# Optimization experiments

Hardware: AMD Instinct MI355X
Metric: run time of the kernel (lower is better)

## Reference

```python
import jax, jax.numpy as jnp
import numpy as np

WS = 8          # window size
NH = 8          # num heads
DIM = 256
HD = DIM // NH  # head dim = 32
SCALE = HD ** -0.5
EPS = 1e-5


def _rel_pos_index(ws):
    # deterministic int index buffer, same math as the torch __init__
    coords = jnp.stack(jnp.meshgrid(jnp.arange(ws), jnp.arange(ws), indexing='ij'))  # [2,ws,ws]
    cf = coords.reshape(2, -1)                     # [2, N]
    rel = cf[:, :, None] - cf[:, None, :]          # [2, N, N]
    return (rel[0] + ws - 1) * (2 * ws - 1) + (rel[1] + ws - 1)  # [N, N]


def _ln(h, g, b):
    m = jnp.mean(h, axis=-1, keepdims=True)
    v = jnp.mean((h - m) ** 2, axis=-1, keepdims=True)
    return (h - m) / jnp.sqrt(v + EPS) * g + b


def setup_inputs() -> dict:
    key = jax.random.key(0)
    ks = jax.random.split(key, 16)
    B_, N, D = 4096, WS * WS, DIM
    s = 0.02
    return {
        'x':      jax.random.normal(ks[0], (B_, N, D), jnp.float32),
        # enhanced qkv: Linear(D,2D) -> LN -> GELU -> Linear(2D,3D)
        'w_qkv1': jax.random.normal(ks[1], (D, 2 * D), jnp.float32) * s,
        'b_qkv1': jnp.zeros((2 * D,), jnp.float32),
        'g_qkv':  jnp.ones((2 * D,), jnp.float32),
        'be_qkv': jnp.zeros((2 * D,), jnp.float32),
        'w_qkv2': jax.random.normal(ks[2], (2 * D, 3 * D), jnp.float32) * s,
        'b_qkv2': jnp.zeros((3 * D,), jnp.float32),
        # relative position bias table [(2*WS-1)^2, NH]
        'rpb':    jax.random.normal(ks[3], ((2 * WS - 1) ** 2, NH), jnp.float32) * s,
        # enhanced proj: Linear(D,2D) -> LN -> GELU -> Linear(2D,D)
        'w_p1':   jax.random.normal(ks[4], (D, 2 * D), jnp.float32) * s,
        'b_p1':   jnp.zeros((2 * D,), jnp.float32),
        'g_p':    jnp.ones((2 * D,), jnp.float32),
        'be_p':   jnp.zeros((2 * D,), jnp.float32),
        'w_p2':   jax.random.normal(ks[5], (2 * D, D), jnp.float32) * s,
        'b_p2':   jnp.zeros((D,), jnp.float32),
    }


def reference(x, w_qkv1, b_qkv1, g_qkv, be_qkv, w_qkv2, b_qkv2, rpb,
              w_p1, b_p1, g_p, be_p, w_p2, b_p2):
    B_, N, C = x.shape
    # enhanced QKV chain: Linear -> LayerNorm -> GELU -> Linear
    h = jax.nn.gelu(_ln(x @ w_qkv1 + b_qkv1, g_qkv, be_qkv), approximate=False)
    qkv = h @ w_qkv2 + b_qkv2                              # [B_, N, 3C]
    qkv = qkv.reshape(B_, N, 3, NH, HD).transpose(2, 0, 3, 1, 4)  # [3, B_, H, N, hd]
    q, k, v = qkv[0], qkv[1], qkv[2]
    attn = jnp.einsum('bhnd,bhmd->bhnm', q * SCALE, k)     # [B_, H, N, N]
    idx = _rel_pos_index(WS)                                # [N, N] int
    bias = rpb[idx.reshape(-1)].reshape(N, N, NH).transpose(2, 0, 1)  # [H, N, N]
    attn = jax.nn.softmax(attn + bias[None], axis=-1)
    out = jnp.einsum('bhnm,bhmd->bhnd', attn, v)           # [B_, H, N, hd]
    out = out.transpose(0, 2, 1, 3).reshape(B_, N, C)
    # enhanced proj chain: Linear -> LayerNorm -> GELU -> Linear
    h = jax.nn.gelu(_ln(out @ w_p1 + b_p1, g_p, be_p), approximate=False)
    return h @ w_p2 + b_p2
```

## Files before the change

### kernel.cpp

```cpp
#include <hip/hip_runtime.h>


typedef __bf16 bf16_t;
typedef __bf16 bf16x8 __attribute__((ext_vector_type(8)));
typedef __bf16 bf16x4 __attribute__((ext_vector_type(4)));
typedef float f32x4 __attribute__((ext_vector_type(4)));

__device__ __forceinline__ f32x4 mfma16(bf16x8 a, bf16x8 b, f32x4 acc) {
  return __builtin_amdgcn_mfma_f32_16x16x32_bf16(a, b, acc, 0, 0, 0);
}

#define SWZ(row, byteoff) ((byteoff) ^ (((row) & 7) << 4))

__device__ __forceinline__ float gelu_f(float v) {
  float e = __expf(v * (1.59576912f + 0.07135482f * v * v));
  return v - v * __builtin_amdgcn_rcpf(1.0f + e);
}

__global__ void wtrans_kernel(const float* __restrict__ src, bf16_t* __restrict__ dst,
                              int kshift, int N, int total) {
  int i = blockIdx.x * 256 + threadIdx.x;
  if (i >= total) return;
  int K = 1 << kshift;
  int k = i & (K - 1);
  int n = i >> kshift;
  dst[i] = (bf16_t)src[(size_t)k * N + n];
}

__global__ void biastab_kernel(const float* __restrict__ rpb, float* __restrict__ bt) {
  int e = blockIdx.x * 256 + threadIdx.x;
  int hd = e >> 12, i = (e >> 6) & 63, j = e & 63;
  int idx = ((i >> 3) - (j >> 3) + 7) * 15 + ((i & 7) - (j & 7) + 7);
  bt[e] = rpb[idx * 8 + hd];
}

__device__ __forceinline__ void gemmT_ln_gelu16(
    const char* bsrc, const bf16_t* __restrict__ wt,
    const float* __restrict__ bias, const float* __restrict__ gamma,
    const float* __restrict__ beta,
    char* dst, int flb, float2* part, int wave, int g, int c)
{
  f32x4 acc[2][4] = {};
#pragma unroll
  for (int kt = 0; kt < 8; ++kt) {
    bf16x8 a[2], b[4];
#pragma unroll
    for (int mt = 0; mt < 2; ++mt)
      a[mt] = *(const bf16x8*)(wt + (size_t)(wave * 32 + mt * 16 + c) * 256 + kt * 32 + g * 8);
#pragma unroll
    for (int nt = 0; nt < 4; ++nt) {
      int T = nt * 16 + c;
      b[nt] = *(const bf16x8*)(bsrc + SWZ(T, T * 512 + kt * 64 + g * 16));
    }
#pragma unroll
    for (int mt = 0; mt < 2; ++mt)
#pragma unroll
      for (int nt = 0; nt < 4; ++nt)
        acc[mt][nt] = mfma16(a[mt], b[nt], acc[mt][nt]);
  }
  float s[4] = {0.f, 0.f, 0.f, 0.f}, ss[4] = {0.f, 0.f, 0.f, 0.f};
#pragma unroll
  for (int mt = 0; mt < 2; ++mt) {
    float4 b4 = *(const float4*)(bias + wave * 32 + mt * 16 + g * 4);
#pragma unroll
    for (int nt = 0; nt < 4; ++nt)
#pragma unroll
      for (int r = 0; r < 4; ++r) {
        float v = acc[mt][nt][r] + ((const float*)&b4)[r];
        acc[mt][nt][r] = v;
        s[nt] += v;
        ss[nt] += v * v;
      }
  }
#pragma unroll
  for (int nt = 0; nt < 4; ++nt) {
    float sv = s[nt], ssv = ss[nt];
    sv += __shfl_xor(sv, 16, 64); ssv += __shfl_xor(ssv, 16, 64);
    sv += __shfl_xor(sv, 32, 64); ssv += __shfl_xor(ssv, 32, 64);
    if (g == 0) part[wave * 64 + nt * 16 + c] = make_float2(sv, ssv);
  }
  __syncthreads();
#pragma unroll
  for (int nt = 0; nt < 4; ++nt) {
    float sv = 0.f, ssv = 0.f;
#pragma unroll
    for (int w = 0; w < 16; ++w) {
      float2 p2 = part[w * 64 + nt * 16 + c];
      sv += p2.x; ssv += p2.y;
    }
    float m = sv * (1.f / 512.f);
    float rstd = rsqrtf(ssv * (1.f / 512.f) - m * m + 1e-5f);
#pragma unroll
    for (int mt = 0; mt < 2; ++mt)
#pragma unroll
      for (int r = 0; r < 4; ++r)
        acc[mt][nt][r] = (acc[mt][nt][r] - m) * rstd;
  }
#pragma unroll
  for (int mt = 0; mt < 2; ++mt) {
    float4 g4 = *(const float4*)(gamma + wave * 32 + mt * 16 + g * 4);
    float4 be4 = *(const float4*)(beta + wave * 32 + mt * 16 + g * 4);
    int f0 = flb + mt * 16 + g * 4;
#pragma unroll
    for (int nt = 0; nt < 4; ++nt) {
      int T = nt * 16 + c;
      bf16x4 h4;
#pragma unroll
      for (int r = 0; r < 4; ++r) {
        float v = acc[mt][nt][r] * ((const float*)&g4)[r] + ((const float*)&be4)[r];
        h4[r] = (bf16_t)gelu_f(v);
      }
      *(bf16x4*)(dst + SWZ(T, T * 512 + f0 * 2)) = h4;
    }
  }
}

__global__ __launch_bounds__(1024, 1) void g1qa_kernel(
    const float* __restrict__ x,
    const bf16_t* __restrict__ w1t, const float* __restrict__ b1,
    const float* __restrict__ gamma1, const float* __restrict__ beta1,
    const bf16_t* __restrict__ w2t, const float* __restrict__ b2,
    const float* __restrict__ bt,
    bf16_t* __restrict__ ao)
{
  __shared__ __align__(16) char sm[98304];
  char* rA = sm;
  char* rB = sm + 32768;
  float2* part = (float2*)(sm + 65536);
  const int tid = threadIdx.x;
  const int wave = tid >> 6, lane = tid & 63;
  const int g = lane >> 4, c = lane & 15;
  const int win = blockIdx.x;

  const float* xw = x + (size_t)win * 16384;
#pragma unroll
  for (int it = 0; it < 4; ++it) {
    int e = it * 4096 + tid * 4;
    float4 v = *(const float4*)(xw + e);
    int row = e >> 8, col = e & 255;
    bf16x4 t4;
    t4[0] = (bf16_t)v.x; t4[1] = (bf16_t)v.y; t4[2] = (bf16_t)v.z; t4[3] = (bf16_t)v.w;
    *(bf16x4*)(rA + SWZ(row, row * 512 + col * 2)) = t4;
  }
  __syncthreads();
  gemmT_ln_gelu16(rA, w1t, b1, gamma1, beta1, (wave < 8) ? rB : rA, (wave & 7) * 32,
                  part, wave, g, c);
  __syncthreads();

  const int hh = wave >> 1, mh = wave & 1;
  bf16x4 vreg[4], qreg[4], kreg[4];
  {
    f32x4 accv[4] = {}, accq[4] = {}, acck[4] = {};
    const bf16_t* wq = w2t + (size_t)(hh * 32 + mh * 16 + c) * 512;
    const bf16_t* wk = wq + (size_t)256 * 512;
    const bf16_t* wv = wq + (size_t)512 * 512;
#pragma unroll
    for (int kt = 0; kt < 16; ++kt) {
      const char* hb = (kt < 8) ? rB : rA;
      const int ko = (kt & 7) * 64 + g * 16;
      bf16x8 av = *(const bf16x8*)(wv + kt * 32 + g * 8);
      bf16x8 aq = *(const bf16x8*)(wq + kt * 32 + g * 8);
      bf16x8 ak = *(const bf16x8*)(wk + kt * 32 + g * 8);
      bf16x8 b[4];
#pragma unroll
      for (int nt = 0; nt < 4; ++nt) {
        int T = nt * 16 + c;
        b[nt] = *(const bf16x8*)(hb + SWZ(T, T * 512 + ko));
      }
#pragma unroll
      for (int nt = 0; nt < 4; ++nt) {
        accv[nt] = mfma16(av, b[nt], accv[nt]);
        accq[nt] = mfma16(aq, b[nt], accq[nt]);
        acck[nt] = mfma16(ak, b[nt], acck[nt]);
      }
    }
    float4 bv4 = *(const float4*)(b2 + 512 + hh * 32 + mh * 16 + g * 4);
    float4 bq4 = *(const float4*)(b2 + hh * 32 + mh * 16 + g * 4);
    float4 bk4 = *(const float4*)(b2 + 256 + hh * 32 + mh * 16 + g * 4);
#pragma unroll
    for (int nt = 0; nt < 4; ++nt)
#pragma unroll
      for (int r = 0; r < 4; ++r) {
        vreg[nt][r] = (bf16_t)(accv[nt][r] + ((const float*)&bv4)[r]);
        qreg[nt][r] = (bf16_t)((accq[nt][r] + ((const float*)&bq4)[r]) * 0.17677669529663687f);
        kreg[nt][r] = (bf16_t)(acck[nt][r] + ((const float*)&bk4)[r]);
      }
  }
  __syncthreads();

  {
    char* qb = sm + hh * 8192;
    const int d0 = mh * 16 + g * 4;
#pragma unroll
    for (int nt = 0; nt < 4; ++nt) {
      int T = nt * 16 + c;
      *(bf16x4*)(qb + SWZ(T, T * 64 + d0 * 2)) = qreg[nt];
      *(bf16x4*)(qb + 4096 + SWZ(T, T * 64 + d0 * 2)) = kreg[nt];
    }
    char* vs = sm + 65536 + hh * 4096;
#pragma unroll
    for (int nt = 0; nt < 4; ++nt) {
      int T = nt * 16 + c;
#pragma unroll
      for (int r = 0; r < 4; ++r) {
        int d = d0 + r;
        *(bf16_t*)(vs + SWZ(d, d * 128 + T * 2)) = vreg[nt][r];
      }
    }
  }
  __syncthreads();

  const int h8 = wave & 7, rowbase = (wave >> 3) * 32;
  char* qb = sm + h8 * 8192;
  char* vslot = sm + 65536 + h8 * 4096;
  const float* btab = bt + h8 * 4096;

  bf16x8 aq[2], bk[4];
#pragma unroll
  for (int mt = 0; mt < 2; ++mt) {
    int t = rowbase + mt * 16 + c;
    aq[mt] = *(const bf16x8*)(qb + SWZ(t, t * 64 + g * 16));
  }
#pragma unroll
  for (int nt = 0; nt < 4; ++nt) {
    int t = nt * 16 + c;
    bk[nt] = *(const bf16x8*)(qb + 4096 + SWZ(t, t * 64 + g * 16));
  }
  float p[2][4][4];
#pragma unroll
  for (int mt = 0; mt < 2; ++mt)
#pragma unroll
    for (int nt = 0; nt < 4; ++nt) {
      f32x4 z = {0.f, 0.f, 0.f, 0.f};
      f32x4 s4 = mfma16(aq[mt], bk[nt], z);
#pragma unroll
      for (int r = 0; r < 4; ++r) {
        int i = rowbase + mt * 16 + g * 4 + r, j = nt * 16 + c;
        p[mt][nt][r] = s4[r] + btab[i * 64 + j];
      }
    }
#pragma unroll
  for (int mt = 0; mt < 2; ++mt)
#pragma unroll
    for (int r = 0; r < 4; ++r) {
      float mx = fmaxf(fmaxf(p[mt][0][r], p[mt][1][r]), fmaxf(p[mt][2][r], p[mt][3][r]));
#pragma unroll
      for (int m = 1; m < 16; m <<= 1) mx = fmaxf(mx, __shfl_xor(mx, m, 64));
      float sum = 0.f;
#pragma unroll
      for (int nt = 0; nt < 4; ++nt) {
        float e = __expf(p[mt][nt][r] - mx);
        p[mt][nt][r] = e; sum += e;
      }
#pragma unroll
      for (int m = 1; m < 16; m <<= 1) sum += __shfl_xor(sum, m, 64);
      float rinv = 1.f / sum;
#pragma unroll
      for (int nt = 0; nt < 4; ++nt) p[mt][nt][r] *= rinv;
    }
  __syncthreads();

#pragma unroll
  for (int mt = 0; mt < 2; ++mt)
#pragma unroll
    for (int nt = 0; nt < 4; ++nt)
#pragma unroll
      for (int r = 0; r < 4; ++r) {
        int i = rowbase + mt * 16 + g * 4 + r, j = nt * 16 + c;
        *(bf16_t*)(qb + SWZ(i, i * 128 + j * 2)) = (bf16_t)p[mt][nt][r];
      }
  asm volatile("s_waitcnt lgkmcnt(0)" ::: "memory");
  f32x4 oacc[2][2] = {};
#pragma unroll
  for (int kp = 0; kp < 2; ++kp) {
    bf16x8 ap[2], bv[2];
#pragma unroll
    for (int mt = 0; mt < 2; ++mt) {
      int t = rowbase + mt * 16 + c;
      ap[mt] = *(const bf16x8*)(qb + SWZ(t, t * 128 + kp * 64 + g * 16));
    }
#pragma unroll
    for (int nt = 0; nt < 2; ++nt) {
      int d = nt * 16 + c;
      bv[nt] = *(const bf16x8*)(vslot + SWZ(d, d * 128 + kp * 64 + g * 16));
    }
#pragma unroll
    for (int mt = 0; mt < 2; ++mt)
#pragma unroll
      for (int nt = 0; nt < 2; ++nt)
        oacc[mt][nt] = mfma16(ap[mt], bv[nt], oacc[mt][nt]);
  }
#pragma unroll
  for (int mt = 0; mt < 2; ++mt)
#pragma unroll
    for (int nt = 0; nt < 2; ++nt)
#pragma unroll
      for (int r = 0; r < 4; ++r) {
        int T = rowbase + mt * 16 + g * 4 + r;
        ao[(size_t)(win * 64 + T) * 256 + h8 * 32 + nt * 16 + c] = (bf16_t)oacc[mt][nt][r];
      }
}

__global__ __launch_bounds__(1024, 1) void g3g4_kernel(
    const bf16_t* __restrict__ ao,
    const bf16_t* __restrict__ wp1t, const float* __restrict__ bp1,
    const float* __restrict__ gp, const float* __restrict__ bep,
    const bf16_t* __restrict__ wp2t, const float* __restrict__ bp2,
    float* __restrict__ out)
{
  __shared__ __align__(16) char sm[73728];
  char* rA = sm;
  char* rB = sm + 32768;
  float2* part = (float2*)(sm + 65536);
  const int tid = threadIdx.x;
  const int wave = tid >> 6, lane = tid & 63;
  const int g = lane >> 4, c = lane & 15;
  const int win = blockIdx.x;

  const bf16_t* aow = ao + (size_t)win * 16384;
#pragma unroll
  for (int it = 0; it < 2; ++it) {
    int e = it * 8192 + tid * 8;
    bf16x8 v = *(const bf16x8*)(aow + e);
    int row = e >> 8, col = e & 255;
    *(bf16x8*)(rA + SWZ(row, row * 512 + col * 2)) = v;
  }
  __syncthreads();
  gemmT_ln_gelu16(rA, wp1t, bp1, gp, bep, (wave < 8) ? rB : rA, (wave & 7) * 32,
                  part, wave, g, c);
  __syncthreads();

  f32x4 acc[4] = {};
#pragma unroll
  for (int kt = 0; kt < 16; ++kt) {
    const char* hb = (kt < 8) ? rB : rA;
    const int ko = (kt & 7) * 64 + g * 16;
    bf16x8 a = *(const bf16x8*)(wp2t + (size_t)(wave * 16 + c) * 512 + kt * 32 + g * 8);
    bf16x8 b[4];
#pragma unroll
    for (int nt = 0; nt < 4; ++nt) {
      int T = nt * 16 + c;
      b[nt] = *(const bf16x8*)(hb + SWZ(T, T * 512 + ko));
    }
#pragma unroll
    for (int nt = 0; nt < 4; ++nt)
      acc[nt] = mfma16(a, b[nt], acc[nt]);
  }
  float* ow = out + (size_t)win * 16384;
  float4 b4 = *(const float4*)(bp2 + wave * 16 + g * 4);
#pragma unroll
  for (int nt = 0; nt < 4; ++nt) {
    int T = nt * 16 + c;
    f32x4 o4;
#pragma unroll
    for (int r = 0; r < 4; ++r) o4[r] = acc[nt][r] + ((const float*)&b4)[r];
    *(f32x4*)(ow + T * 256 + wave * 16 + g * 4) = o4;
  }
}

extern "C" void kernel_launch(void* const* d_in, const int* in_sizes, int n_in,
                              void* d_out, int out_size, void* d_ws, size_t ws_size,
                              hipStream_t stream) {
  const float* x   = (const float*)d_in[0];
  const float* w1  = (const float*)d_in[1];
  const float* b1  = (const float*)d_in[2];
  const float* g1  = (const float*)d_in[3];
  const float* be1 = (const float*)d_in[4];
  const float* w2  = (const float*)d_in[5];
  const float* b2  = (const float*)d_in[6];
  const float* rpb = (const float*)d_in[7];
  const float* wp1 = (const float*)d_in[8];
  const float* bp1 = (const float*)d_in[9];
  const float* gp  = (const float*)d_in[10];
  const float* bep = (const float*)d_in[11];
  const float* wp2 = (const float*)d_in[12];
  const float* bp2 = (const float*)d_in[13];
  float* out = (float*)d_out;
  char* ws = (char*)d_ws;
  bf16_t* w1t  = (bf16_t*)(ws + 0);
  bf16_t* w2t  = (bf16_t*)(ws + 262144);
  bf16_t* wp1t = (bf16_t*)(ws + 1048576);
  bf16_t* wp2t = (bf16_t*)(ws + 1310720);
  float*  bt   = (float*)(ws + 1572864);
  bf16_t* ao   = (bf16_t*)(ws + 2097152);

  wtrans_kernel<<<512, 256, 0, stream>>>(w1, w1t, 8, 512, 131072);
  wtrans_kernel<<<1536, 256, 0, stream>>>(w2, w2t, 9, 768, 393216);
  wtrans_kernel<<<512, 256, 0, stream>>>(wp1, wp1t, 8, 512, 131072);
  wtrans_kernel<<<512, 256, 0, stream>>>(wp2, wp2t, 9, 256, 131072);
  biastab_kernel<<<128, 256, 0, stream>>>(rpb, bt);

  g1qa_kernel<<<4096, 1024, 0, stream>>>(x, w1t, b1, g1, be1, w2t, b2, bt, ao);
  g3g4_kernel<<<4096, 1024, 0, stream>>>(ao, wp1t, bp1, gp, bep, wp2t, bp2, out);
}
```

Before: 1.104 ms.

## Fuse attention and projection kernels into one per-window mega kernel

Merges the QKV+attention kernel and the projection-chain kernel into a single kernel per window. The attention output now stays in LDS (a new 32KB region) instead of round-tripping through global memory as bf16, and one launch is dropped. LDS use per block rises from 96KB to 128KB, which still allows one 1024-thread block per CU but may limit occupancy or scheduling flexibility.

```diff
diff --git a/kernel.cpp b/kernel.cpp
--- a/kernel.cpp
+++ b/kernel.cpp
@@ -115,18 +115,22 @@
   }
 }
 
-__global__ __launch_bounds__(1024, 1) void g1qa_kernel(
+__global__ __launch_bounds__(1024, 1) void mega_kernel(
     const float* __restrict__ x,
     const bf16_t* __restrict__ w1t, const float* __restrict__ b1,
     const float* __restrict__ gamma1, const float* __restrict__ beta1,
     const bf16_t* __restrict__ w2t, const float* __restrict__ b2,
     const float* __restrict__ bt,
-    bf16_t* __restrict__ ao)
+    const bf16_t* __restrict__ wp1t, const float* __restrict__ bp1,
+    const float* __restrict__ gp, const float* __restrict__ bep,
+    const bf16_t* __restrict__ wp2t, const float* __restrict__ bp2,
+    float* __restrict__ out)
 {
-  __shared__ __align__(16) char sm[98304];
+  __shared__ __align__(16) char sm[131072];
   char* rA = sm;
   char* rB = sm + 32768;
   float2* part = (float2*)(sm + 65536);
+  char* aoS = sm + 98304;
   const int tid = threadIdx.x;
   const int wave = tid >> 6, lane = tid & 63;
   const int g = lane >> 4, c = lane & 15;
@@ -210,151 +214,131 @@
   }
   __syncthreads();
 
-  const int h8 = wave & 7, rowbase = (wave >> 3) * 32;
-  char* qb = sm + h8 * 8192;
-  char* vslot = sm + 65536 + h8 * 4096;
-  const float* btab = bt + h8 * 4096;
-
-  bf16x8 aq[2], bk[4];
-#pragma unroll
-  for (int mt = 0; mt < 2; ++mt) {
-    int t = rowbase + mt * 16 + c;
-    aq[mt] = *(const bf16x8*)(qb + SWZ(t, t * 64 + g * 16));
-  }
-#pragma unroll
-  for (int nt = 0; nt < 4; ++nt) {
-    int t = nt * 16 + c;
-    bk[nt] = *(const bf16x8*)(qb + 4096 + SWZ(t, t * 64 + g * 16));
-  }
-  float p[2][4][4];
-#pragma unroll
-  for (int mt = 0; mt < 2; ++mt)
-#pragma unroll
-    for (int nt = 0; nt < 4; ++nt) {
-      f32x4 z = {0.f, 0.f, 0.f, 0.f};
-      f32x4 s4 = mfma16(aq[mt], bk[nt], z);
-#pragma unroll
-      for (int r = 0; r < 4; ++r) {
-        int i = rowbase + mt * 16 + g * 4 + r, j = nt * 16 + c;
-        p[mt][nt][r] = s4[r] + btab[i * 64 + j];
-      }
-    }
-#pragma unroll
-  for (int mt = 0; mt < 2; ++mt)
-#pragma unroll
-    for (int r = 0; r < 4; ++r) {
-      float mx = fmaxf(fmaxf(p[mt][0][r], p[mt][1][r]), fmaxf(p[mt][2][r], p[mt][3][r]));
-#pragma unroll
-      for (int m = 1; m < 16; m <<= 1) mx = fmaxf(mx, __shfl_xor(mx, m, 64));
-      float sum = 0.f;
-#pragma unroll
-      for (int nt = 0; nt < 4; ++nt) {
-        float e = __expf(p[mt][nt][r] - mx);
-        p[mt][nt][r] = e; sum += e;
-      }
-#pragma unroll
-      for (int m = 1; m < 16; m <<= 1) sum += __shfl_xor(sum, m, 64);
-      float rinv = 1.f / sum;
-#pragma unroll
-      for (int nt = 0; nt < 4; ++nt) p[mt][nt][r] *= rinv;
-    }
-  __syncthreads();
-
-#pragma unroll
-  for (int mt = 0; mt < 2; ++mt)
-#pragma unroll
-    for (int nt = 0; nt < 4; ++nt)
-#pragma unroll
-      for (int r = 0; r < 4; ++r) {
-        int i = rowbase + mt * 16 + g * 4 + r, j = nt * 16 + c;
-        *(bf16_t*)(qb + SWZ(i, i * 128 + j * 2)) = (bf16_t)p[mt][nt][r];
-      }
-  asm volatile("s_waitcnt lgkmcnt(0)" ::: "memory");
-  f32x4 oacc[2][2] = {};
-#pragma unroll
-  for (int kp = 0; kp < 2; ++kp) {
-    bf16x8 ap[2], bv[2];
+  {
+    const int h8 = wave & 7, rowbase = (wave >> 3) * 32;
+    char* qb = sm + h8 * 8192;
+    char* vslot = sm + 65536 + h8 * 4096;
+    const float* btab = bt + h8 * 4096;
+
+    bf16x8 aq[2], bk[4];
 #pragma unroll
     for (int mt = 0; mt < 2; ++mt) {
       int t = rowbase + mt * 16 + c;
-      ap[mt] = *(const bf16x8*)(qb + SWZ(t, t * 128 + kp * 64 + g * 16));
-    }
-#pragma unroll
-    for (int nt = 0; nt < 2; ++nt) {
-      int d = nt * 16 + c;
-      bv[nt] = *(const bf16x8*)(vslot + SWZ(d, d * 128 + kp * 64 + g * 16));
+      aq[mt] = *(const bf16x8*)(qb + SWZ(t, t * 64 + g * 16));
+    }
+#pragma unroll
+    for (int nt = 0; nt < 4; ++nt) {
+      int t = nt * 16 + c;
+      bk[nt] = *(const bf16x8*)(qb + 4096 + SWZ(t, t * 64 + g * 16));
+    }
+    float p[2][4][4];
+#pragma unroll
+    for (int mt = 0; mt < 2; ++mt)
+#pragma unroll
+      for (int nt = 0; nt < 4; ++nt) {
+        f32x4 z = {0.f, 0.f, 0.f, 0.f};
+        f32x4 s4 = mfma16(aq[mt], bk[nt], z);
+#pragma unroll
+        for (int r = 0; r < 4; ++r) {
+          int i = rowbase + mt * 16 + g * 4 + r, j = nt * 16 + c;
+          p[mt][nt][r] = s4[r] + btab[i * 64 + j];
+        }
+      }
+#pragma unroll
+    for (int mt = 0; mt < 2; ++mt)
+#pragma unroll
+      for (int r = 0; r < 4; ++r) {
+        float mx = fmaxf(fmaxf(p[mt][0][r], p[mt][1][r]), fmaxf(p[mt][2][r], p[mt][3][r]));
+#pragma unroll
+        for (int m = 1; m < 16; m <<= 1) mx = fmaxf(mx, __shfl_xor(mx, m, 64));
+        float sum = 0.f;
+#pragma unroll
+        for (int nt = 0; nt < 4; ++nt) {
+          float e = __expf(p[mt][nt][r] - mx);
+          p[mt][nt][r] = e; sum += e;
+        }
+#pragma unroll
+        for (int m = 1; m < 16; m <<= 1) sum += __shfl_xor(sum, m, 64);
+        float rinv = 1.f / sum;
+#pragma unroll
+        for (int nt = 0; nt < 4; ++nt) p[mt][nt][r] *= rinv;
+      }
+    __syncthreads();
+
+#pragma unroll
+    for (int mt = 0; mt < 2; ++mt)
+#pragma unroll
+      for (int nt = 0; nt < 4; ++nt)
+#pragma unroll
+        for (int r = 0; r < 4; ++r) {
+          int i = rowbase + mt * 16 + g * 4 + r, j = nt * 16 + c;
+          *(bf16_t*)(qb + SWZ(i, i * 128 + j * 2)) = (bf16_t)p[mt][nt][r];
+        }
+    asm volatile("s_waitcnt lgkmcnt(0)" ::: "memory");
+    f32x4 oacc[2][2] = {};
+#pragma unroll
+    for (int kp = 0; kp < 2; ++kp) {
+      bf16x8 ap[2], bv[2];
+#pragma unroll
+      for (int mt = 0; mt < 2; ++mt) {
+        int t = rowbase + mt * 16 + c;
+        ap[mt] = *(const bf16x8*)(qb + SWZ(t, t * 128 + kp * 64 + g * 16));
+      }
+#pragma unroll
+      for (int nt = 0; nt < 2; ++nt) {
+        int d = nt * 16 + c;
+        bv[nt] = *(const bf16x8*)(vslot + SWZ(d, d * 128 + kp * 64 + g * 16));
+      }
+#pragma unroll
+      for (int mt = 0; mt < 2; ++mt)
+#pragma unroll
+        for (int nt = 0; nt < 2; ++nt)
+          oacc[mt][nt] = mfma16(ap[mt], bv[nt], oacc[mt][nt]);
     }
 #pragma unroll
     for (int mt = 0; mt < 2; ++mt)
 #pragma unroll
       for (int nt = 0; nt < 2; ++nt)
-        oacc[mt][nt] = mfma16(ap[mt], bv[nt], oacc[mt][nt]);
-  }
-#pragma unroll
-  for (int mt = 0; mt < 2; ++mt)
-#pragma unroll
-    for (int nt = 0; nt < 2; ++nt)
-#pragma unroll
-      for (int r = 0; r < 4; ++r) {
-        int T = rowbase + mt * 16 + g * 4 + r;
-        ao[(size_t)(win * 64 + T) * 256 + h8 * 32 + nt * 16 + c] = (bf16_t)oacc[mt][nt][r];
-      }
-}
-
-__global__ __launch_bounds__(1024, 1) void g3g4_kernel(
-    const bf16_t* __restrict__ ao,
-    const bf16_t* __restrict__ wp1t, const float* __restrict__ bp1,
-    const float* __restrict__ gp, const float* __restrict__ bep,
-    const bf16_t* __restrict__ wp2t, const float* __restrict__ bp2,
-    float* __restrict__ out)
-{
-  __shared__ __align__(16) char sm[73728];
-  char* rA = sm;
-  char* rB = sm + 32768;
-  float2* part = (float2*)(sm + 65536);
-  const int tid = threadIdx.x;
-  const int wave = tid >> 6, lane = tid & 63;
-  const int g = lane >> 4, c = lane & 15;
-  const int win = blockIdx.x;
-
-  const bf16_t* aow = ao + (size_t)win * 16384;
-#pragma unroll
-  for (int it = 0; it < 2; ++it) {
-    int e = it * 8192 + tid * 8;
-    bf16x8 v = *(const bf16x8*)(aow + e);
-    int row = e >> 8, col = e & 255;
-    *(bf16x8*)(rA + SWZ(row, row * 512 + col * 2)) = v;
-  }
-  __syncthreads();
-  gemmT_ln_gelu16(rA, wp1t, bp1, gp, bep, (wave < 8) ? rB : rA, (wave & 7) * 32,
+#pragma unroll
+        for (int r = 0; r < 4; ++r) {
+          int T = rowbase + mt * 16 + g * 4 + r;
+          int f = h8 * 32 + nt * 16 + c;
+          *(bf16_t*)(aoS + SWZ(T, T * 512 + f * 2)) = (bf16_t)oacc[mt][nt][r];
+        }
+  }
+  __syncthreads();
+
+  gemmT_ln_gelu16(aoS, wp1t, bp1, gp, bep, (wave < 8) ? rB : rA, (wave & 7) * 32,
                   part, wave, g, c);
   __syncthreads();
 
-  f32x4 acc[4] = {};
-#pragma unroll
-  for (int kt = 0; kt < 16; ++kt) {
-    const char* hb = (kt < 8) ? rB : rA;
-    const int ko = (kt & 7) * 64 + g * 16;
-    bf16x8 a = *(const bf16x8*)(wp2t + (size_t)(wave * 16 + c) * 512 + kt * 32 + g * 8);
-    bf16x8 b[4];
-#pragma unroll
-    for (int nt = 0; nt < 4; ++nt) {
-      int T = nt * 16 + c;
-      b[nt] = *(const bf16x8*)(hb + SWZ(T, T * 512 + ko));
-    }
-#pragma unroll
-    for (int nt = 0; nt < 4; ++nt)
-      acc[nt] = mfma16(a, b[nt], acc[nt]);
-  }
-  float* ow = out + (size_t)win * 16384;
-  float4 b4 = *(const float4*)(bp2 + wave * 16 + g * 4);
-#pragma unroll
-  for (int nt = 0; nt < 4; ++nt) {
-    int T = nt * 16 + c;
-    f32x4 o4;
-#pragma unroll
-    for (int r = 0; r < 4; ++r) o4[r] = acc[nt][r] + ((const float*)&b4)[r];
-    *(f32x4*)(ow + T * 256 + wave * 16 + g * 4) = o4;
+  {
+    f32x4 acc[4] = {};
+#pragma unroll
+    for (int kt = 0; kt < 16; ++kt) {
+      const char* hb = (kt < 8) ? rB : rA;
+      const int ko = (kt & 7) * 64 + g * 16;
+      bf16x8 a = *(const bf16x8*)(wp2t + (size_t)(wave * 16 + c) * 512 + kt * 32 + g * 8);
+      bf16x8 b[4];
+#pragma unroll
+      for (int nt = 0; nt < 4; ++nt) {
+        int T = nt * 16 + c;
+        b[nt] = *(const bf16x8*)(hb + SWZ(T, T * 512 + ko));
+      }
+#pragma unroll
+      for (int nt = 0; nt < 4; ++nt)
+        acc[nt] = mfma16(a, b[nt], acc[nt]);
+    }
+    float* ow = out + (size_t)win * 16384;
+    float4 b4 = *(const float4*)(bp2 + wave * 16 + g * 4);
+#pragma unroll
+    for (int nt = 0; nt < 4; ++nt) {
+      int T = nt * 16 + c;
+      f32x4 o4;
+#pragma unroll
+      for (int r = 0; r < 4; ++r) o4[r] = acc[nt][r] + ((const float*)&b4)[r];
+      *(f32x4*)(ow + T * 256 + wave * 16 + g * 4) = o4;
+    }
   }
 }
 
@@ -382,7 +366,6 @@
   bf16_t* wp1t = (bf16_t*)(ws + 1048576);
   bf16_t* wp2t = (bf16_t*)(ws + 1310720);
   float*  bt   = (float*)(ws + 1572864);
-  bf16_t* ao   = (bf16_t*)(ws + 2097152);
 
   wtrans_kernel<<<512, 256, 0, stream>>>(w1, w1t, 8, 512, 131072);
   wtrans_kernel<<<1536, 256, 0, stream>>>(w2, w2t, 9, 768, 393216);
@@ -390,6 +373,6 @@
   wtrans_kernel<<<512, 256, 0, stream>>>(wp2, wp2t, 9, 256, 131072);
   biastab_kernel<<<128, 256, 0, stream>>>(rpb, bt);
 
-  g1qa_kernel<<<4096, 1024, 0, stream>>>(x, w1t, b1, g1, be1, w2t, b2, bt, ao);
-  g3g4_kernel<<<4096, 1024, 0, stream>>>(ao, wp1t, bp1, gp, bep, wp2t, bp2, out);
-}
+  mega_kernel<<<4096, 1024, 0, stream>>>(x, w1t, b1, g1, be1, w2t, b2, bt,
+                                         wp1t, bp1, gp, bep, wp2t, bp2, out);
+}
```

Measured after the change: 1.184 ms. 7.2% more time.

## Merge prep kernels, drop a barrier in QKV epilogue, retile final GEMM

Applied to the files above, without the earlier changes.

Folds the four weight-transpose launches and the bias-table launch into a single prep kernel to cut launch overhead. In the attention kernel, shared memory grows to 160KB so the Q/K/V results can be written directly into a fresh region, which removes a __syncthreads and the register staging of q/k/v. The final projection GEMM is retiled so each wave computes a 32x32 output tile instead of 16x64, reusing A and B fragments across two MFMAs each. The larger LDS footprint is still within one 1024-thread block per CU.

```diff
diff --git a/kernel.cpp b/kernel.cpp
--- a/kernel.cpp
+++ b/kernel.cpp
@@ -17,21 +17,42 @@
   return v - v * __builtin_amdgcn_rcpf(1.0f + e);
 }
 
-__global__ void wtrans_kernel(const float* __restrict__ src, bf16_t* __restrict__ dst,
-                              int kshift, int N, int total) {
+__global__ void prep_kernel(const float* __restrict__ w1, const float* __restrict__ w2,
+                            const float* __restrict__ wp1, const float* __restrict__ wp2,
+                            const float* __restrict__ rpb,
+                            bf16_t* __restrict__ w1t, bf16_t* __restrict__ w2t,
+                            bf16_t* __restrict__ wp1t, bf16_t* __restrict__ wp2t,
+                            float* __restrict__ bt) {
   int i = blockIdx.x * 256 + threadIdx.x;
-  if (i >= total) return;
-  int K = 1 << kshift;
-  int k = i & (K - 1);
-  int n = i >> kshift;
-  dst[i] = (bf16_t)src[(size_t)k * N + n];
-}
-
-__global__ void biastab_kernel(const float* __restrict__ rpb, float* __restrict__ bt) {
-  int e = blockIdx.x * 256 + threadIdx.x;
-  int hd = e >> 12, i = (e >> 6) & 63, j = e & 63;
-  int idx = ((i >> 3) - (j >> 3) + 7) * 15 + ((i & 7) - (j & 7) + 7);
-  bt[e] = rpb[idx * 8 + hd];
+  if (i < 131072) {
+    int k = i & 255, n = i >> 8;
+    w1t[i] = (bf16_t)w1[k * 512 + n];
+    return;
+  }
+  i -= 131072;
+  if (i < 393216) {
+    int k = i & 511, n = i >> 9;
+    w2t[i] = (bf16_t)w2[k * 768 + n];
+    return;
+  }
+  i -= 393216;
+  if (i < 131072) {
+    int k = i & 255, n = i >> 8;
+    wp1t[i] = (bf16_t)wp1[k * 512 + n];
+    return;
+  }
+  i -= 131072;
+  if (i < 131072) {
+    int k = i & 511, n = i >> 9;
+    wp2t[i] = (bf16_t)wp2[k * 256 + n];
+    return;
+  }
+  i -= 131072;
+  if (i < 32768) {
+    int hd = i >> 12, r = (i >> 6) & 63, j = i & 63;
+    int idx = ((r >> 3) - (j >> 3) + 7) * 15 + ((r & 7) - (j & 7) + 7);
+    bt[i] = rpb[idx * 8 + hd];
+  }
 }
 
 __device__ __forceinline__ void gemmT_ln_gelu16(
@@ -123,7 +144,7 @@
     const float* __restrict__ bt,
     bf16_t* __restrict__ ao)
 {
-  __shared__ __align__(16) char sm[98304];
+  __shared__ __align__(16) char sm[163840];
   char* rA = sm;
   char* rB = sm + 32768;
   float2* part = (float2*)(sm + 65536);
@@ -148,7 +169,6 @@
   __syncthreads();
 
   const int hh = wave >> 1, mh = wave & 1;
-  bf16x4 vreg[4], qreg[4], kreg[4];
   {
     f32x4 accv[4] = {}, accq[4] = {}, acck[4] = {};
     const bf16_t* wq = w2t + (size_t)(hh * 32 + mh * 16 + c) * 512;
@@ -177,42 +197,33 @@
     float4 bv4 = *(const float4*)(b2 + 512 + hh * 32 + mh * 16 + g * 4);
     float4 bq4 = *(const float4*)(b2 + hh * 32 + mh * 16 + g * 4);
     float4 bk4 = *(const float4*)(b2 + 256 + hh * 32 + mh * 16 + g * 4);
-#pragma unroll
-    for (int nt = 0; nt < 4; ++nt)
-#pragma unroll
-      for (int r = 0; r < 4; ++r) {
-        vreg[nt][r] = (bf16_t)(accv[nt][r] + ((const float*)&bv4)[r]);
-        qreg[nt][r] = (bf16_t)((accq[nt][r] + ((const float*)&bq4)[r]) * 0.17677669529663687f);
-        kreg[nt][r] = (bf16_t)(acck[nt][r] + ((const float*)&bk4)[r]);
-      }
-  }
-  __syncthreads();
-
-  {
-    char* qb = sm + hh * 8192;
+    char* qb = sm + 65536 + hh * 8192;
+    char* vs = sm + 131072 + hh * 4096;
     const int d0 = mh * 16 + g * 4;
 #pragma unroll
     for (int nt = 0; nt < 4; ++nt) {
       int T = nt * 16 + c;
-      *(bf16x4*)(qb + SWZ(T, T * 64 + d0 * 2)) = qreg[nt];
-      *(bf16x4*)(qb + 4096 + SWZ(T, T * 64 + d0 * 2)) = kreg[nt];
-    }
-    char* vs = sm + 65536 + hh * 4096;
-#pragma unroll
-    for (int nt = 0; nt < 4; ++nt) {
-      int T = nt * 16 + c;
+      bf16x4 q4, k4;
+#pragma unroll
+      for (int r = 0; r < 4; ++r) {
+        q4[r] = (bf16_t)((accq[nt][r] + ((const float*)&bq4)[r]) * 0.17677669529663687f);
+        k4[r] = (bf16_t)(acck[nt][r] + ((const float*)&bk4)[r]);
+      }
+      *(bf16x4*)(qb + SWZ(T, T * 64 + d0 * 2)) = q4;
+      *(bf16x4*)(qb + 4096 + SWZ(T, T * 64 + d0 * 2)) = k4;
 #pragma unroll
       for (int r = 0; r < 4; ++r) {
         int d = d0 + r;
-        *(bf16_t*)(vs + SWZ(d, d * 128 + T * 2)) = vreg[nt][r];
+        *(bf16_t*)(vs + SWZ(d, d * 128 + T * 2)) =
+            (bf16_t)(accv[nt][r] + ((const float*)&bv4)[r]);
       }
     }
   }
   __syncthreads();
 
   const int h8 = wave & 7, rowbase = (wave >> 3) * 32;
-  char* qb = sm + h8 * 8192;
-  char* vslot = sm + 65536 + h8 * 4096;
+  char* qb = sm + 65536 + h8 * 8192;
+  char* vslot = sm + 131072 + h8 * 4096;
   const float* btab = bt + h8 * 4096;
 
   bf16x8 aq[2], bk[4];
@@ -330,31 +341,41 @@
                   part, wave, g, c);
   __syncthreads();
 
-  f32x4 acc[4] = {};
-#pragma unroll
-  for (int kt = 0; kt < 16; ++kt) {
-    const char* hb = (kt < 8) ? rB : rA;
-    const int ko = (kt & 7) * 64 + g * 16;
-    bf16x8 a = *(const bf16x8*)(wp2t + (size_t)(wave * 16 + c) * 512 + kt * 32 + g * 8);
-    bf16x8 b[4];
-#pragma unroll
-    for (int nt = 0; nt < 4; ++nt) {
-      int T = nt * 16 + c;
-      b[nt] = *(const bf16x8*)(hb + SWZ(T, T * 512 + ko));
-    }
-#pragma unroll
-    for (int nt = 0; nt < 4; ++nt)
-      acc[nt] = mfma16(a, b[nt], acc[nt]);
-  }
-  float* ow = out + (size_t)win * 16384;
-  float4 b4 = *(const float4*)(bp2 + wave * 16 + g * 4);
-#pragma unroll
-  for (int nt = 0; nt < 4; ++nt) {
-    int T = nt * 16 + c;
-    f32x4 o4;
-#pragma unroll
-    for (int r = 0; r < 4; ++r) o4[r] = acc[nt][r] + ((const float*)&b4)[r];
-    *(f32x4*)(ow + T * 256 + wave * 16 + g * 4) = o4;
+  {
+    const int f0 = (wave & 7) * 32, t0 = (wave >> 3) * 32;
+    f32x4 acc[2][2] = {};
+#pragma unroll
+    for (int kt = 0; kt < 16; ++kt) {
+      const char* hb = (kt < 8) ? rB : rA;
+      const int ko = (kt & 7) * 64 + g * 16;
+      bf16x8 a[2], b[2];
+#pragma unroll
+      for (int mt = 0; mt < 2; ++mt)
+        a[mt] = *(const bf16x8*)(wp2t + (size_t)(f0 + mt * 16 + c) * 512 + kt * 32 + g * 8);
+#pragma unroll
+      for (int nt = 0; nt < 2; ++nt) {
+        int T = t0 + nt * 16 + c;
+        b[nt] = *(const bf16x8*)(hb + SWZ(T, T * 512 + ko));
+      }
+#pragma unroll
+      for (int mt = 0; mt < 2; ++mt)
+#pragma unroll
+        for (int nt = 0; nt < 2; ++nt)
+          acc[mt][nt] = mfma16(a[mt], b[nt], acc[mt][nt]);
+    }
+    float* ow = out + (size_t)win * 16384;
+#pragma unroll
+    for (int mt = 0; mt < 2; ++mt) {
+      float4 b4 = *(const float4*)(bp2 + f0 + mt * 16 + g * 4);
+#pragma unroll
+      for (int nt = 0; nt < 2; ++nt) {
+        int T = t0 + nt * 16 + c;
+        f32x4 o4;
+#pragma unroll
+        for (int r = 0; r < 4; ++r) o4[r] = acc[mt][nt][r] + ((const float*)&b4)[r];
+        *(f32x4*)(ow + T * 256 + f0 + mt * 16 + g * 4) = o4;
+      }
+    }
   }
 }
 
@@ -384,11 +405,8 @@
   float*  bt   = (float*)(ws + 1572864);
   bf16_t* ao   = (bf16_t*)(ws + 2097152);
 
-  wtrans_kernel<<<512, 256, 0, stream>>>(w1, w1t, 8, 512, 131072);
-  wtrans_kernel<<<1536, 256, 0, stream>>>(w2, w2t, 9, 768, 393216);
-  wtrans_kernel<<<512, 256, 0, stream>>>(wp1, wp1t, 8, 512, 131072);
-  wtrans_kernel<<<512, 256, 0, stream>>>(wp2, wp2t, 9, 256, 131072);
-  biastab_kernel<<<128, 256, 0, stream>>>(rpb, bt);
+  prep_kernel<<<3200, 256, 0, stream>>>(w1, w2, wp1, wp2, rpb,
+                                        w1t, w2t, wp1t, wp2t, bt);
 
   g1qa_kernel<<<4096, 1024, 0, stream>>>(x, w1t, b1, g1, be1, w2t, b2, bt, ao);
   g3g4_kernel<<<4096, 1024, 0, stream>>>(ao, wp1t, bp1, gp, bep, wp2t, bp2, out);
```

After: 1.209 ms. +9.5%, slower.
